# Optimization experiments

Measured on AMD Instinct MI355X. Metric: run time of the kernel, lower is better.

The kernel has to match this reference:

```python
import jax, jax.numpy as jnp
import numpy as np

N_HEAD = 16

def setup_inputs() -> dict:
    key = jax.random.key(0)
    k1, k2, k3 = jax.random.split(key, 3)
    B, T, D = 1, 2048, 1024
    x = jax.random.normal(k1, (B, T, D), dtype=jnp.float32)
    # torch Linear(d, 3d, bias=False): y = x @ W.T with W [3d, d]; store transposed [d, 3d]
    W_qkv = jax.random.normal(k2, (D, 3 * D), dtype=jnp.float32) * 0.02
    W_o = jax.random.normal(k3, (D, D), dtype=jnp.float32) * 0.02
    return {"x": x, "W_qkv": W_qkv, "W_o": W_o}

def reference(x, W_qkv, W_o):
    B, T, D = x.shape
    H = N_HEAD
    hd = D // H
    qkv = (x @ W_qkv).reshape(B, T, 3, H, hd)
    q, k, v = qkv[:, :, 0], qkv[:, :, 1], qkv[:, :, 2]  # [B, T, H, hd]
    scale = 1.0 / np.sqrt(hd).astype(np.float32)
    # The per-chunk loop with growing context + mask is exactly dense causal attention.
    att = jnp.einsum('bqhd,bkhd->bhqk', q, k) * scale  # [B, H, T, T]
    causal = jnp.tril(jnp.ones((T, T), dtype=bool))
    att = jnp.where(causal[None, None], att, jnp.finfo(att.dtype).min)
    att = jax.nn.softmax(att, axis=-1)
    y = jnp.einsum('bhqk,bkhd->bqhd', att, v).reshape(B, T, D)
    return y @ W_o
```

## Files before the change

### kernel.cpp

```cpp
#include <hip/hip_runtime.h>
#include <hip/hip_bf16.h>


using u16 = unsigned short;
typedef __attribute__((ext_vector_type(8))) __bf16 bf16x8;
typedef __attribute__((ext_vector_type(8))) unsigned short u16x8;
typedef __attribute__((ext_vector_type(4))) float f32x4;

__device__ __forceinline__ u16 f2bf(float f) {
  union { float f; unsigned u; } v; v.f = f;
  unsigned r = v.u + 0x7FFFu + ((v.u >> 16) & 1u);
  return (u16)(r >> 16);
}

__device__ __forceinline__ float bf2f(u16 b) {
  union { unsigned u; float f; } v; v.u = ((unsigned)b) << 16;
  return v.f;
}

__device__ __forceinline__ unsigned cvt_pk_bf16(float lo, float hi) {
  unsigned r;
  asm("v_cvt_pk_bf16_f32 %0, %1, %2" : "=v"(r) : "v"(lo), "v"(hi));
  return r;
}

__device__ __forceinline__ void gload_lds16(const void* g, void* l) {
  __builtin_amdgcn_global_load_lds((const __attribute__((address_space(1))) void*)g,
                                   (__attribute__((address_space(3))) void*)l, 16, 0, 0);
}

__device__ __forceinline__ f32x4 mfma16(bf16x8 a, bf16x8 b, f32x4 c) {
  return __builtin_amdgcn_mfma_f32_16x16x32_bf16(a, b, c, 0, 0, 0);
}

__global__ __launch_bounds__(256) void prep_kernel(const float* __restrict__ x,
                                                   const float* __restrict__ Wqkv,
                                                   const float* __restrict__ Wo,
                                                   u16* __restrict__ xb,
                                                   u16* __restrict__ WqkvT,
                                                   u16* __restrict__ WoT) {
  __shared__ u16 tile[32][33];
  const int b = blockIdx.x;
  if (b < 1024) {
    const int i = (b * 256 + threadIdx.x) * 8;
    float4 a = *(const float4*)(x + i);
    float4 c = *(const float4*)(x + i + 4);
    u16x8 r;
    r[0] = f2bf(a.x); r[1] = f2bf(a.y); r[2] = f2bf(a.z); r[3] = f2bf(a.w);
    r[4] = f2bf(c.x); r[5] = f2bf(c.y); r[6] = f2bf(c.z); r[7] = f2bf(c.w);
    *(u16x8*)(xb + i) = r;
    return;
  }
  const float* in; u16* out; int R, C, bx, by;
  if (b < 1024 + 3072) {
    const int tb = b - 1024;
    in = Wqkv; out = WqkvT; R = 1024; C = 3072; bx = tb % 96; by = tb / 96;
  } else {
    const int tb = b - 4096;
    in = Wo; out = WoT; R = 1024; C = 1024; bx = tb % 32; by = tb / 32;
  }
  const int c0 = bx * 32, r0 = by * 32;
  const int tx = threadIdx.x & 31, ty = threadIdx.x >> 5;
#pragma unroll
  for (int rr = ty; rr < 32; rr += 8)
    tile[rr][tx] = f2bf(in[(size_t)(r0 + rr) * C + (c0 + tx)]);
  __syncthreads();
#pragma unroll
  for (int rr = ty; rr < 32; rr += 8)
    out[(size_t)(c0 + rr) * R + (r0 + tx)] = tile[tx][rr];
}

template <int BN, typename OutT>
__global__ __launch_bounds__(256) void gemm_bt_kernel(const u16* __restrict__ A,
                                                      const u16* __restrict__ Bt,
                                                      OutT* __restrict__ C,
                                                      int M, int N, int K) {
  constexpr int BM = 128, BK = 32;
  constexpr int NFR = BN / 32;
  __shared__ u16 As[2][BM * BK];
  __shared__ u16 Bs[2][BN * BK];
  const int tid = threadIdx.x;
  const int lane = tid & 63, wid = tid >> 6;
  const int l16 = lane & 15, l4 = lane >> 4;
  const int wr = (wid >> 1) * 64, wc = (wid & 1) * (BN / 2);
  const long bm = (long)blockIdx.x * BM, bn = (long)blockIdx.y * BN;

  f32x4 acc[4][NFR] = {};
  const int KT = K / BK;

  auto stage = [&](int buf, int kt) {
    const int k0 = kt * BK;
#pragma unroll
    for (int half = 0; half < 2; ++half) {
      int t = half * 256 + tid;
      int row = t >> 2, c8 = (t & 3) << 3;
      gload_lds16(A + (bm + row) * (size_t)K + k0 + c8, &As[buf][row * BK + c8]);
    }
#pragma unroll
    for (int half = 0; half < 2; ++half) {
      int t = half * 256 + tid;
      if (t < BN * 4) {
        int row = t >> 2, c8 = (t & 3) << 3;
        gload_lds16(Bt + (bn + row) * (size_t)K + k0 + c8, &Bs[buf][row * BK + c8]);
      }
    }
  };

  stage(0, 0);
  __syncthreads();
  int cur = 0;
  for (int kt = 0; kt < KT; ++kt) {
    if (kt + 1 < KT) stage(cur ^ 1, kt + 1);
    bf16x8 af[4], bfr[NFR];
#pragma unroll
    for (int m = 0; m < 4; ++m)
      af[m] = *(const bf16x8*)&As[cur][(wr + m * 16 + l16) * BK + l4 * 8];
#pragma unroll
    for (int n = 0; n < NFR; ++n)
      bfr[n] = *(const bf16x8*)&Bs[cur][(wc + n * 16 + l16) * BK + l4 * 8];
#pragma unroll
    for (int m = 0; m < 4; ++m)
#pragma unroll
      for (int n = 0; n < NFR; ++n)
        acc[m][n] = mfma16(af[m], bfr[n], acc[m][n]);
    __syncthreads();
    cur ^= 1;
  }

#pragma unroll
  for (int m = 0; m < 4; ++m) {
    const long row0 = bm + wr + m * 16 + l4 * 4;
#pragma unroll
    for (int n = 0; n < NFR; ++n) {
      const long col = bn + wc + n * 16 + l16;
#pragma unroll
      for (int j = 0; j < 4; ++j) {
        float v = acc[m][n][j];
        if constexpr (sizeof(OutT) == 2)
          C[(row0 + j) * N + col] = (OutT)f2bf(v);
        else
          C[(row0 + j) * N + col] = (OutT)v;
      }
    }
  }
}

__global__ __launch_bounds__(256, 4) void attn_kernel(const u16* __restrict__ qkv,
                                                      u16* __restrict__ opart,
                                                      float2* __restrict__ ml, int S) {
  constexpr int W = 3072;
  const int p = blockIdx.x, h = blockIdx.y, s = blockIdx.z;
  const int tid = threadIdx.x, wid = tid >> 6, lane = tid & 63;
  const int l16 = lane & 15, l4 = lane >> 4;
  const int w0 = (33 * s) / S, w1 = (33 * (s + 1)) / S;

  __shared__ u16 Ks[2][64 * 64];
  __shared__ u16 Vt[2][64][72];

  constexpr float cl2 = 0.125f * 1.44269504f;
  const int vpos = (lane & 32) | ((lane & 12) << 1) | ((lane & 16) >> 2) | (lane & 3);

  auto stageK = [&](int buf, int k0) {
#pragma unroll
    for (int half = 0; half < 2; ++half) {
      int t = half * 256 + tid;
      int row = t >> 3, chunk = t & 7;
      int srcChunk = chunk ^ (row & 7);
      gload_lds16(qkv + (size_t)(k0 + row) * W + 1024 + h * 64 + srcChunk * 8,
                  &Ks[buf][t * 8]);
    }
  };

  bool didA = false, didB = false;
  int w = w0;
  while (w < w1) {
    const bool isA = (w <= p);
    const int qt = isA ? p : 31 - p;
    const int wend = isA ? ((w1 < p + 1) ? w1 : (p + 1)) : w1;
    const int kvb = isA ? 0 : p + 1;
    if (isA) didA = true; else didB = true;

    const int q0 = qt * 64;
    const int qr = q0 + wid * 16 + l16;

    const u16* qrow = qkv + (size_t)(q0 + wid * 16 + l16) * W + h * 64;
    const bf16x8 qa0 = *(const bf16x8*)(qrow + l4 * 8);
    const bf16x8 qa1 = *(const bf16x8*)(qrow + 32 + l4 * 8);

    f32x4 o[4] = {};
    float mrow = -3e38f, lsum = 0.f;

    {
      const int k0 = (w - kvb) * 64;
      stageK(0, k0);
      const u16* vsrc = qkv + (size_t)(k0 + lane) * W + 2048 + h * 64 + wid * 16;
      u16x8 a = *(const u16x8*)vsrc;
      u16x8 b = *(const u16x8*)(vsrc + 8);
#pragma unroll
      for (int i = 0; i < 8; ++i) Vt[0][wid * 16 + i][vpos] = a[i];
#pragma unroll
      for (int i = 0; i < 8; ++i) Vt[0][wid * 16 + 8 + i][vpos] = b[i];
      __syncthreads();
    }

    int cur = 0;
    for (; w < wend; ++w) {
      const int kv = w - kvb;
      const int k0 = kv * 64;
      const bool pf = (w + 1 < wend);

      u16x8 va, vb2;
      if (pf) {
        stageK(cur ^ 1, k0 + 64);
        const u16* vsrc = qkv + (size_t)(k0 + 64 + lane) * W + 2048 + h * 64 + wid * 16;
        va = *(const u16x8*)vsrc;
        vb2 = *(const u16x8*)(vsrc + 8);
      }

      f32x4 sv[4];
#pragma unroll
      for (int nb = 0; nb < 4; ++nb) {
        const int krow = nb * 16 + l16;
        const char* kbase = (const char*)&Ks[cur][0] + krow * 128;
        const int swz = (krow & 7) << 4;
        bf16x8 kb0 = *(const bf16x8*)(kbase + ((l4 * 16) ^ swz));
        bf16x8 kb1 = *(const bf16x8*)(kbase + ((64 + l4 * 16) ^ swz));
        f32x4 z = {0.f, 0.f, 0.f, 0.f};
        z = mfma16(kb0, qa0, z);
        sv[nb] = mfma16(kb1, qa1, z);
      }

      float pv[4][4];
      const bool diag = (kv == qt);
#pragma unroll
      for (int nb = 0; nb < 4; ++nb)
#pragma unroll
        for (int j = 0; j < 4; ++j) {
          float v = sv[nb][j] * cl2;
          if (diag) {
            const int key = k0 + nb * 16 + l4 * 4 + j;
            v = (key <= qr) ? v : -3e38f;
          }
          pv[nb][j] = v;
        }

      float rmax = -3e38f;
#pragma unroll
      for (int nb = 0; nb < 4; ++nb)
#pragma unroll
        for (int j = 0; j < 4; ++j) rmax = fmaxf(rmax, pv[nb][j]);
      rmax = fmaxf(rmax, __shfl_xor(rmax, 16));
      rmax = fmaxf(rmax, __shfl_xor(rmax, 32));

      const float mnew = fmaxf(mrow, rmax);
      if (__any(mnew > mrow)) {
        const float sc = exp2f(mrow - mnew);
        mrow = mnew;
        lsum *= sc;
#pragma unroll
        for (int db = 0; db < 4; ++db)
#pragma unroll
          for (int j = 0; j < 4; ++j) o[db][j] *= sc;
      }

#pragma unroll
      for (int nb = 0; nb < 4; ++nb)
#pragma unroll
        for (int j = 0; j < 4; ++j) {
          const float e = exp2f(pv[nb][j] - mrow);
          pv[nb][j] = e;
          lsum += e;
        }

      uint4 pk0, pk1;
      pk0.x = cvt_pk_bf16(pv[0][0], pv[0][1]);
      pk0.y = cvt_pk_bf16(pv[0][2], pv[0][3]);
      pk0.z = cvt_pk_bf16(pv[1][0], pv[1][1]);
      pk0.w = cvt_pk_bf16(pv[1][2], pv[1][3]);
      pk1.x = cvt_pk_bf16(pv[2][0], pv[2][1]);
      pk1.y = cvt_pk_bf16(pv[2][2], pv[2][3]);
      pk1.z = cvt_pk_bf16(pv[3][0], pv[3][1]);
      pk1.w = cvt_pk_bf16(pv[3][2], pv[3][3]);

#pragma unroll
      for (int db = 0; db < 4; ++db) {
        bf16x8 va0 = *(const bf16x8*)&Vt[cur][db * 16 + l16][l4 * 8];
        bf16x8 va1 = *(const bf16x8*)&Vt[cur][db * 16 + l16][32 + l4 * 8];
        o[db] = mfma16(va0, *(const bf16x8*)&pk0, o[db]);
        o[db] = mfma16(va1, *(const bf16x8*)&pk1, o[db]);
      }

      if (pf) {
#pragma unroll
        for (int i = 0; i < 8; ++i) Vt[cur ^ 1][wid * 16 + i][vpos] = va[i];
#pragma unroll
        for (int i = 0; i < 8; ++i) Vt[cur ^ 1][wid * 16 + 8 + i][vpos] = vb2[i];
      }
      __syncthreads();
      cur ^= 1;
    }

    float lrow = lsum;
    lrow += __shfl_xor(lrow, 16);
    lrow += __shfl_xor(lrow, 32);
    {
      const size_t q = q0 + wid * 16 + l16;
      u16* orow = opart + ((q * 16 + h) * S + s) * 64;
#pragma unroll
      for (int db = 0; db < 4; ++db) {
        uint2 w2;
        w2.x = cvt_pk_bf16(o[db][0], o[db][1]);
        w2.y = cvt_pk_bf16(o[db][2], o[db][3]);
        *(uint2*)&orow[db * 16 + l4 * 4] = w2;
      }
      if (l4 == 0)
        ml[(q * 16 + h) * S + s] = make_float2(mrow, lrow);
    }
  }

  if (!didA && tid < 64)
    ml[((size_t)(p * 64 + tid) * 16 + h) * S + s] = make_float2(-3e38f, 0.f);
  if (!didB && tid < 64)
    ml[((size_t)((31 - p) * 64 + tid) * 16 + h) * S + s] = make_float2(-3e38f, 0.f);
}

__global__ __launch_bounds__(256) void combine_kernel(const u16* __restrict__ opart,
                                                      const float2* __restrict__ ml,
                                                      u16* __restrict__ y, int S) {
  const int p = blockIdx.x * 4 + (threadIdx.x >> 6);
  const int d = threadIdx.x & 63;
  float M = -3e38f;
  for (int s = 0; s < S; ++s) M = fmaxf(M, ml[(size_t)p * S + s].x);
  float num = 0.f, den = 0.f;
  for (int s = 0; s < S; ++s) {
    const float2 m2 = ml[(size_t)p * S + s];
    const float w = exp2f(m2.x - M);
    num += w * bf2f(opart[((size_t)p * S + s) * 64 + d]);
    den += w * m2.y;
  }
  const int q = p >> 4, h = p & 15;
  y[(size_t)q * 1024 + h * 64 + d] = f2bf(num / den);
}

extern "C" void kernel_launch(void* const* d_in, const int* in_sizes, int n_in,
                              void* d_out, int out_size, void* d_ws, size_t ws_size,
                              hipStream_t stream) {
  constexpr int T = 2048, D = 1024;
  const float* x    = (const float*)d_in[0];
  const float* Wqkv = (const float*)d_in[1];
  const float* Wo   = (const float*)d_in[2];
  float* out = (float*)d_out;

  u16* xb    = (u16*)d_ws;
  u16* WqkvT = xb + (size_t)T * D;
  u16* WoT   = WqkvT + (size_t)3 * D * D;
  u16* qkv   = WoT + (size_t)D * D;
  u16* yb    = qkv + (size_t)T * 3 * D;

  const size_t baseB = (size_t)(T * D + 3 * D * D + D * D + T * 3 * D + T * D) * 2;
  auto needB = [&](int S) {
    return baseB + (size_t)T * 16 * S * 64 * 2 + (size_t)T * 16 * S * 8;
  };
  const int S = (ws_size >= needB(4)) ? 4 : 2;
  u16*    opart = (u16*)((char*)d_ws + baseB);
  float2* ml    = (float2*)((char*)d_ws + baseB + (size_t)T * 16 * S * 64 * 2);

  prep_kernel<<<1024 + 3072 + 1024, 256, 0, stream>>>(x, Wqkv, Wo, xb, WqkvT, WoT);

  gemm_bt_kernel<96, u16><<<dim3(T / 128, 3 * D / 96), 256, 0, stream>>>(
      xb, WqkvT, qkv, T, 3 * D, D);

  attn_kernel<<<dim3(16, 16, S), 256, 0, stream>>>(qkv, opart, ml, S);
  combine_kernel<<<T * 16 / 4, 256, 0, stream>>>(opart, ml, yb, S);

  gemm_bt_kernel<64, float><<<dim3(T / 128, D / 64), 256, 0, stream>>>(
      yb, WoT, out, T, D, D);
}
```

Before: 99.55 us.

## Pre-transpose V globally and triple-buffer K with direct V register loads

Adds a separate kernel that writes V transposed and key-permuted into a workspace buffer. The attention kernel can then load V MFMA fragments straight from global memory into registers, with no LDS staging or scalar transposed LDS writes. K staging moves to a three-deep LDS ring with explicit vmcnt waits and a raw s_barrier in place of __syncthreads. In exchange it adds one kernel launch and an extra read and write pass over V, and the V global loads sit on the critical path of each iteration.

```diff
diff --git a/kernel.cpp b/kernel.cpp
--- a/kernel.cpp
+++ b/kernel.cpp
@@ -31,6 +31,10 @@
 
 __device__ __forceinline__ f32x4 mfma16(bf16x8 a, bf16x8 b, f32x4 c) {
   return __builtin_amdgcn_mfma_f32_16x16x32_bf16(a, b, c, 0, 0, 0);
+}
+
+__device__ __forceinline__ int sigma64(int key) {
+  return (key & 32) | ((key & 12) << 1) | ((key & 16) >> 2) | (key & 3);
 }
 
 __global__ __launch_bounds__(256) void prep_kernel(const float* __restrict__ x,
@@ -70,6 +74,22 @@
     out[(size_t)(c0 + rr) * R + (r0 + tx)] = tile[tx][rr];
 }
 
+__global__ __launch_bounds__(256) void vtrans_kernel(const u16* __restrict__ qkv,
+                                                     u16* __restrict__ vT) {
+  __shared__ u16 tile[32][33];
+  const int key0 = blockIdx.x * 32, c0 = blockIdx.y * 32;
+  const int tx = threadIdx.x & 31, ty = threadIdx.x >> 5;
+#pragma unroll
+  for (int rr = ty; rr < 32; rr += 8)
+    tile[rr][tx] = qkv[(size_t)(key0 + rr) * 3072 + 2048 + c0 + tx];
+  __syncthreads();
+  const int key = key0 + tx;
+  const int pos = (key & ~63) | sigma64(key & 63);
+#pragma unroll
+  for (int rr = ty; rr < 32; rr += 8)
+    vT[(size_t)(c0 + rr) * 2048 + pos] = tile[tx][rr];
+}
+
 template <int BN, typename OutT>
 __global__ __launch_bounds__(256) void gemm_bt_kernel(const u16* __restrict__ A,
                                                       const u16* __restrict__ Bt,
@@ -146,6 +166,7 @@
 }
 
 __global__ __launch_bounds__(256, 4) void attn_kernel(const u16* __restrict__ qkv,
+                                                      const u16* __restrict__ vT,
                                                       u16* __restrict__ opart,
                                                       float2* __restrict__ ml, int S) {
   constexpr int W = 3072;
@@ -154,11 +175,9 @@
   const int l16 = lane & 15, l4 = lane >> 4;
   const int w0 = (33 * s) / S, w1 = (33 * (s + 1)) / S;
 
-  __shared__ u16 Ks[2][64 * 64];
-  __shared__ u16 Vt[2][64][72];
+  __shared__ u16 Ks[3][64 * 64];
 
   constexpr float cl2 = 0.125f * 1.44269504f;
-  const int vpos = (lane & 32) | ((lane & 12) << 1) | ((lane & 16) >> 2) | (lane & 3);
 
   auto stageK = [&](int buf, int k0) {
 #pragma unroll
@@ -190,31 +209,27 @@
     f32x4 o[4] = {};
     float mrow = -3e38f, lsum = 0.f;
 
-    {
-      const int k0 = (w - kvb) * 64;
-      stageK(0, k0);
-      const u16* vsrc = qkv + (size_t)(k0 + lane) * W + 2048 + h * 64 + wid * 16;
-      u16x8 a = *(const u16x8*)vsrc;
-      u16x8 b = *(const u16x8*)(vsrc + 8);
-#pragma unroll
-      for (int i = 0; i < 8; ++i) Vt[0][wid * 16 + i][vpos] = a[i];
-#pragma unroll
-      for (int i = 0; i < 8; ++i) Vt[0][wid * 16 + 8 + i][vpos] = b[i];
-      __syncthreads();
-    }
+    __builtin_amdgcn_sched_barrier(0);
+    stageK(0, (w - kvb) * 64);
+    if (w + 1 < wend) {
+      stageK(1, (w - kvb) * 64 + 64);
+      asm volatile("s_waitcnt vmcnt(2)" ::: "memory");
+    } else {
+      asm volatile("s_waitcnt vmcnt(0)" ::: "memory");
+    }
+    __builtin_amdgcn_s_barrier();
 
     int cur = 0;
     for (; w < wend; ++w) {
       const int kv = w - kvb;
       const int k0 = kv * 64;
-      const bool pf = (w + 1 < wend);
-
-      u16x8 va, vb2;
-      if (pf) {
-        stageK(cur ^ 1, k0 + 64);
-        const u16* vsrc = qkv + (size_t)(k0 + 64 + lane) * W + 2048 + h * 64 + wid * 16;
-        va = *(const u16x8*)vsrc;
-        vb2 = *(const u16x8*)(vsrc + 8);
+
+      bf16x8 vfr[8];
+#pragma unroll
+      for (int db = 0; db < 4; ++db) {
+        const u16* vrow = vT + (size_t)(h * 64 + db * 16 + l16) * 2048 + k0;
+        vfr[2 * db]     = *(const bf16x8*)(vrow + l4 * 8);
+        vfr[2 * db + 1] = *(const bf16x8*)(vrow + 32 + l4 * 8);
       }
 
       f32x4 sv[4];
@@ -284,20 +299,15 @@
 
 #pragma unroll
       for (int db = 0; db < 4; ++db) {
-        bf16x8 va0 = *(const bf16x8*)&Vt[cur][db * 16 + l16][l4 * 8];
-        bf16x8 va1 = *(const bf16x8*)&Vt[cur][db * 16 + l16][32 + l4 * 8];
-        o[db] = mfma16(va0, *(const bf16x8*)&pk0, o[db]);
-        o[db] = mfma16(va1, *(const bf16x8*)&pk1, o[db]);
-      }
-
-      if (pf) {
-#pragma unroll
-        for (int i = 0; i < 8; ++i) Vt[cur ^ 1][wid * 16 + i][vpos] = va[i];
-#pragma unroll
-        for (int i = 0; i < 8; ++i) Vt[cur ^ 1][wid * 16 + 8 + i][vpos] = vb2[i];
-      }
-      __syncthreads();
-      cur ^= 1;
+        o[db] = mfma16(vfr[2 * db], *(const bf16x8*)&pk0, o[db]);
+        o[db] = mfma16(vfr[2 * db + 1], *(const bf16x8*)&pk1, o[db]);
+      }
+
+      __builtin_amdgcn_sched_barrier(0);
+      if (w + 2 < wend) stageK((cur + 2) % 3, k0 + 128);
+      asm volatile("s_waitcnt vmcnt(2)" ::: "memory");
+      __builtin_amdgcn_s_barrier();
+      cur = (cur + 1) % 3;
     }
 
     float lrow = lsum;
@@ -356,8 +366,10 @@
   u16* WoT   = WqkvT + (size_t)3 * D * D;
   u16* qkv   = WoT + (size_t)D * D;
   u16* yb    = qkv + (size_t)T * 3 * D;
-
-  const size_t baseB = (size_t)(T * D + 3 * D * D + D * D + T * 3 * D + T * D) * 2;
+  u16* vT    = yb + (size_t)T * D;
+
+  const size_t baseB =
+      (size_t)(T * D + 3 * D * D + D * D + T * 3 * D + T * D + T * D) * 2;
   auto needB = [&](int S) {
     return baseB + (size_t)T * 16 * S * 64 * 2 + (size_t)T * 16 * S * 8;
   };
@@ -370,7 +382,9 @@
   gemm_bt_kernel<96, u16><<<dim3(T / 128, 3 * D / 96), 256, 0, stream>>>(
       xb, WqkvT, qkv, T, 3 * D, D);
 
-  attn_kernel<<<dim3(16, 16, S), 256, 0, stream>>>(qkv, opart, ml, S);
+  vtrans_kernel<<<dim3(T / 32, D / 32), 256, 0, stream>>>(qkv, vT);
+
+  attn_kernel<<<dim3(16, 16, S), 256, 0, stream>>>(qkv, vT, opart, ml, S);
   combine_kernel<<<T * 16 / 4, 256, 0, stream>>>(opart, ml, yb, S);
 
   gemm_bt_kernel<64, float><<<dim3(T / 128, D / 64), 256, 0, stream>>>(
```

Measured after the change: 111.7 us. 12.2% more time.
